# Kernel tuning notes

Hardware: AMD Instinct MI355X
Metric: run time of the kernel (lower is better)

Reference implementation:

```python
import jax, jax.numpy as jnp
import numpy as np

K = 3  # kernel size


def _bilinear_sample(x, px, py):
    """Bilinear sample x:[b,c,h,w] at pixel coords px,py:[b,t,h,w].
    Zeros padding, align_corners=True semantics (coords are raw pixel coords).
    Returns [b,c,t,h,w]."""
    b, c, h, w = x.shape
    x0 = jnp.floor(px)
    y0 = jnp.floor(py)
    wx1 = px - x0
    wx0 = 1.0 - wx1
    wy1 = py - y0
    wy0 = 1.0 - wy1
    xf = x.reshape(b, c, h * w)

    def gather(xi, yi):
        valid = (xi >= 0) & (xi <= w - 1) & (yi >= 0) & (yi <= h - 1)
        xi_c = jnp.clip(xi, 0, w - 1).astype(jnp.int32)
        yi_c = jnp.clip(yi, 0, h - 1).astype(jnp.int32)
        idx = (yi_c * w + xi_c).reshape(b, 1, -1)  # [b,1,t*h*w]
        v = jnp.take_along_axis(xf, idx, axis=2).reshape(b, c, *xi.shape[1:])
        return v * valid[:, None].astype(x.dtype)

    out = (gather(x0, y0) * (wx0 * wy0)[:, None]
           + gather(x0 + 1, y0) * (wx1 * wy0)[:, None]
           + gather(x0, y0 + 1) * (wx0 * wy1)[:, None]
           + gather(x0 + 1, y0 + 1) * (wx1 * wy1)[:, None])
    return out


def setup_inputs() -> dict:
    key = jax.random.key(0)
    k1, k2, k3 = jax.random.split(key, 3)
    b, c, h, w = 4, 64, 128, 128
    out_c = 64
    x = jax.random.normal(k1, (b, c, h, w), dtype=jnp.float32)
    offset = jax.random.normal(k2, (b, 2 * K * K, h, w), dtype=jnp.float32)
    weight = jax.random.normal(k3, (out_c, c, K, K), dtype=jnp.float32) * 0.05
    bias = jnp.zeros((out_c,), dtype=jnp.float32)
    return {"x": x, "offset": offset, "weight": weight, "bias": bias}


def reference(x, offset, weight, bias):
    b, c, h, w = x.shape
    kk = K * K
    # base integer grid (x along width, y along height)
    yy, xx = jnp.meshgrid(jnp.arange(h, dtype=x.dtype), jnp.arange(w, dtype=x.dtype), indexing='ij')
    off = offset.reshape(b, kk, 2, h, w)
    # grid_sample with align_corners=True inverts the module's normalization,
    # so effective sampling coords are simply base + offset in pixel space.
    px = xx[None, None] + off[:, :, 0]  # [b,kk,h,w]
    py = yy[None, None] + off[:, :, 1]
    sampled = _bilinear_sample(x, px, py)  # [b,c,kk,h,w]
    w2 = weight.reshape(weight.shape[0], c, kk)  # [o,c,kk]
    out = jnp.einsum('oct,bcthw->bohw', w2, sampled)
    return out + bias[None, :, None, None]
```

## Files before the change

### kernel.cpp

```cpp
#include <hip/hip_runtime.h>
#include <cstddef>

#define BH 4
#define CH 64
#define OH 64
#define HH 128
#define WW 128
#define KK 9
#define HW (HH * WW)

#define HX 4
#define HYT 4
#define TW 25
#define TH 12
#define NREC (TW * TH)
#define NCHUNK (NREC * 8)

typedef __attribute__((ext_vector_type(8))) short short8;
typedef __attribute__((ext_vector_type(4))) float f32x4;
typedef __attribute__((ext_vector_type(2))) float f32x2;
typedef __attribute__((ext_vector_type(4))) unsigned int uint4v;
typedef __attribute__((ext_vector_type(8))) unsigned short ushort8v;

__device__ __forceinline__ unsigned short f2bf(float f) {
    unsigned u = __float_as_uint(f);
    u += 0x7fffu + ((u >> 16) & 1u);
    return (unsigned short)(u >> 16);
}
__device__ __forceinline__ f32x2 bf2x2(unsigned d) {
    f32x2 r;
    r.x = __uint_as_float(d << 16);
    r.y = __uint_as_float(d & 0xffff0000u);
    return r;
}
__device__ __forceinline__ unsigned pack_bf2(f32x2 v) {
    unsigned u0 = __float_as_uint(v.x);
    u0 += 0x7fffu + ((u0 >> 16) & 1u);
    unsigned u1 = __float_as_uint(v.y);
    u1 += 0x7fffu + ((u1 >> 16) & 1u);
    return __builtin_amdgcn_perm(u1, u0, 0x07060302);
}
__device__ __forceinline__ uint4v combine4(uint4v c00, uint4v c10, uint4v c01, uint4v c11,
                                           float w00, float w10, float w01, float w11) {
    f32x2 W00 = {w00, w00}, W10 = {w10, w10}, W01 = {w01, w01}, W11 = {w11, w11};
    uint4v r;
#pragma unroll
    for (int j = 0; j < 4; ++j) {
        f32x2 s = W00 * bf2x2(c00[j]) + W10 * bf2x2(c10[j])
                + W01 * bf2x2(c01[j]) + W11 * bf2x2(c11[j]);
        r[j] = pack_bf2(s);
    }
    return r;
}

__global__ __launch_bounds__(256) void dcl_prep(const float* __restrict__ x,
                                                const float* __restrict__ wgt,
                                                unsigned short* __restrict__ xt,
                                                unsigned short* __restrict__ wtb) {
    if (blockIdx.x < 1024) {
        __shared__ float tile[64][68];
        int chunk = blockIdx.x;
        int b = chunk >> 8;
        int hw0 = (chunk & 255) * 64;
        int tid = threadIdx.x;
        int cg = tid >> 4;
        int tx4 = (tid & 15) * 4;
        const float* xb = x + (size_t)b * CH * HW + hw0;
#pragma unroll
        for (int pass = 0; pass < 4; ++pass) {
            int c = pass * 16 + cg;
            float4 v = *(const float4*)(xb + (size_t)c * HW + tx4);
            *(float4*)&tile[c][tx4] = v;
        }
        __syncthreads();
        unsigned short* xtb = xt + ((size_t)b << 20) + (size_t)hw0 * CH;
        int c8 = (tid & 7) * 8;
        int p0 = tid >> 3;
#pragma unroll
        for (int it = 0; it < 2; ++it) {
            int pxl = p0 + it * 32;
            ushort8v v;
#pragma unroll
            for (int j = 0; j < 8; ++j) v[j] = f2bf(tile[c8 + j][pxl]);
            *(ushort8v*)(xtb + (size_t)pxl * CH + c8) = v;
        }
    } else {
        int idx = (blockIdx.x - 1024) * 256 + threadIdx.x;
        int j  = idx & 7;
        int l  = (idx >> 3) & 63;
        int nt = (idx >> 9) & 3;
        int ks = idx >> 11;
        int k = ks * 32 + ((l >> 4) * 8) + j;
        int n = nt * 16 + (l & 15);
        int c = k & 63;
        int t = k >> 6;
        wtb[idx] = f2bf(wgt[(n * CH + c) * KK + t]);
    }
}

__global__ __launch_bounds__(256, 4) void dcl_main(
        const unsigned short* __restrict__ xt,
        const float* __restrict__ offset,
        const unsigned short* __restrict__ wtb,
        const float* __restrict__ bias,
        float* __restrict__ out) {
    __shared__ __align__(16) int smem[NREC * 32];
    int tid = threadIdx.x;
    int lane = tid & 63;
    int wave = tid >> 6;

    int b  = blockIdx.x >> 8;
    int t8 = blockIdx.x & 255;
    int x0 = (t8 & 7) << 4;
    int y0 = (t8 >> 3) << 2;
    int m = lane & 15;
    int quad = lane >> 4;
    int qoff = quad * 16;
    int y = y0 + wave;
    int pm = x0 + m;

    const char* xtb = (const char*)xt;
    const char* xim = xtb + (((size_t)b << 14) << 7);
    const float* ob = offset + (((size_t)(b * 18)) << 14) + (y << 7) + pm;
    float pxf = (float)pm;
    float pyf = (float)y;

    float oxv[9], oyv[9];
#pragma unroll
    for (int t = 0; t < 9; ++t) {
        oxv[t] = ob[(size_t)(2 * t) << 14];
        oyv[t] = ob[(size_t)(2 * t + 1) << 14];
    }

    uint4v* sv = (uint4v*)smem;
#pragma unroll
    for (int i = 0; i < 10; ++i) {
        int id = tid + i * 256;
        if (id < NCHUNK) {
            int p = id >> 3, sub = id & 7;
            int r = p / TW, col = p - r * TW;
            int sy = min(max(y0 - HYT + r, 0), HH - 1);
            int sx = min(max(x0 - HX + col, 0), WW - 1);
            uint4v v = *(const uint4v*)(xim + (((sy << 7) + sx) << 7) + (sub << 4));
            sv[p * 8 + ((sub + (p & 7)) & 7)] = v;
        }
    }

    f32x4 acc[4];
#pragma unroll
    for (int i = 0; i < 4; ++i) acc[i] = (f32x4)(0.f);

    const short8* bfrags = (const short8*)wtb;

    __syncthreads();

#pragma unroll
    for (int t = 0; t < 9; ++t) {
        float fx = pxf + oxv[t];
        float fy = pyf + oyv[t];
        float x0f = floorf(fx), y0f = floorf(fy);
        float wx1 = fx - x0f, wy1 = fy - y0f;
        float wx0 = 1.0f - wx1, wy0 = 1.0f - wy1;
        int ix0 = (int)x0f, iy0 = (int)y0f;
        int ix1 = ix0 + 1, iy1 = iy0 + 1;
        bool vx0 = (unsigned)ix0 < (unsigned)WW;
        bool vx1 = (unsigned)ix1 < (unsigned)WW;
        bool vy0 = (unsigned)iy0 < (unsigned)HH;
        bool vy1 = (unsigned)iy1 < (unsigned)HH;
        float w00 = (vx0 && vy0) ? wx0 * wy0 : 0.0f;
        float w10 = (vx1 && vy0) ? wx1 * wy0 : 0.0f;
        float w01 = (vx0 && vy1) ? wx0 * wy1 : 0.0f;
        float w11 = (vx1 && vy1) ? wx1 * wy1 : 0.0f;
        int cx0 = min(max(ix0, 0), WW - 1), cx1 = min(max(ix1, 0), WW - 1);
        int cy0 = min(max(iy0, 0), HH - 1), cy1 = min(max(iy1, 0), HH - 1);

        int lc0 = cx0 - x0 + HX, lc1 = cx1 - x0 + HX;
        int lr0 = cy0 - y0 + HYT, lr1 = cy1 - y0 + HYT;
        bool oof = ((unsigned)lc0 > (TW - 1)) | ((unsigned)lc1 > (TW - 1)) |
                   ((unsigned)lr0 > (TH - 1)) | ((unsigned)lr1 > (TH - 1));
        int sc0 = min(max(lc0, 0), TW - 1), sc1 = min(max(lc1, 0), TW - 1);
        int sr0 = min(max(lr0, 0), TH - 1), sr1 = min(max(lr1, 0), TH - 1);
        int p00 = sr0 * TW + sc0, p10 = sr0 * TW + sc1;
        int p01 = sr1 * TW + sc0, p11 = sr1 * TW + sc1;

        uint4v c00a = sv[p00 * 8 + ((quad + (p00 & 7)) & 7)];
        uint4v c00b = sv[p00 * 8 + ((quad + 4 + (p00 & 7)) & 7)];
        uint4v c10a = sv[p10 * 8 + ((quad + (p10 & 7)) & 7)];
        uint4v c10b = sv[p10 * 8 + ((quad + 4 + (p10 & 7)) & 7)];
        uint4v c01a = sv[p01 * 8 + ((quad + (p01 & 7)) & 7)];
        uint4v c01b = sv[p01 * 8 + ((quad + 4 + (p01 & 7)) & 7)];
        uint4v c11a = sv[p11 * 8 + ((quad + (p11 & 7)) & 7)];
        uint4v c11b = sv[p11 * 8 + ((quad + 4 + (p11 & 7)) & 7)];

        if (__builtin_expect(oof, 0)) {
            int base = b << 14;
            int o00 = ((base + (cy0 << 7) + cx0) << 7) + qoff;
            int o10 = ((base + (cy0 << 7) + cx1) << 7) + qoff;
            int o01 = ((base + (cy1 << 7) + cx0) << 7) + qoff;
            int o11 = ((base + (cy1 << 7) + cx1) << 7) + qoff;
            c00a = *(const uint4v*)(xtb + o00);
            c00b = *(const uint4v*)(xtb + o00 + 64);
            c10a = *(const uint4v*)(xtb + o10);
            c10b = *(const uint4v*)(xtb + o10 + 64);
            c01a = *(const uint4v*)(xtb + o01);
            c01b = *(const uint4v*)(xtb + o01 + 64);
            c11a = *(const uint4v*)(xtb + o11);
            c11b = *(const uint4v*)(xtb + o11 + 64);
        }

        uint4v ra = combine4(c00a, c10a, c01a, c11a, w00, w10, w01, w11);
        uint4v rb = combine4(c00b, c10b, c01b, c11b, w00, w10, w01, w11);
        short8 aa = __builtin_bit_cast(short8, ra);
        short8 ab = __builtin_bit_cast(short8, rb);

        int ks = 2 * t;
#pragma unroll
        for (int nt = 0; nt < 4; ++nt)
            acc[nt] = __builtin_amdgcn_mfma_f32_16x16x32_bf16(
                aa, bfrags[(ks * 4 + nt) * 64 + lane], acc[nt], 0, 0, 0);
#pragma unroll
        for (int nt = 0; nt < 4; ++nt)
            acc[nt] = __builtin_amdgcn_mfma_f32_16x16x32_bf16(
                ab, bfrags[((ks + 1) * 4 + nt) * 64 + lane], acc[nt], 0, 0, 0);
    }

    __syncthreads();
    float* o_w = (float*)smem + wave * 1040;
#pragma unroll
    for (int nt = 0; nt < 4; ++nt)
#pragma unroll
        for (int reg = 0; reg < 4; ++reg)
            o_w[(quad * 4 + reg) * 65 + nt * 16 + m] = acc[nt][reg];
    __syncthreads();

    const float* os = (const float*)smem;
#pragma unroll
    for (int j = tid; j < 64 * 64; j += 256) {
        int o = j >> 6;
        int p = j & 63;
        int row = p >> 4, xx = p & 15;
        float v = os[row * 1040 + xx * 65 + o] + bias[o];
        out[(((size_t)(b * OH + o)) << 14) + ((y0 + row) << 7) + x0 + xx] = v;
    }
}

extern "C" void kernel_launch(void* const* d_in, const int* in_sizes, int n_in,
                              void* d_out, int out_size, void* d_ws, size_t ws_size,
                              hipStream_t stream) {
    const float* x      = (const float*)d_in[0];
    const float* offset = (const float*)d_in[1];
    const float* weight = (const float*)d_in[2];
    const float* bias   = (const float*)d_in[3];
    float* out = (float*)d_out;

    unsigned short* xt  = (unsigned short*)d_ws;
    unsigned short* wtb = (unsigned short*)((char*)d_ws + (size_t)BH * HW * CH * 2);

    dcl_prep<<<1024 + 144, 256, 0, stream>>>(x, weight, xt, wtb);
    dcl_main<<<(BH * HW) / 64, 256, 0, stream>>>(xt, offset, wtb, bias, out);
}
```

Baseline: 101.3 us.

## Process two output rows per wave to reuse weight fragments and halo tile

Each block now covers a 16x8 pixel tile instead of 16x4, and each wave computes two rows with two accumulator sets. Every loaded B (weight) fragment feeds twice as many MFMAs, and the shared-memory halo tile grows from 12 to 16 rows, so halo overhead per output pixel drops. The per-pixel gather is factored into a helper, and offsets are loaded inside the tap loop rather than preloaded. In exchange, register and LDS pressure rise (launch bounds drop to 3 blocks per CU) and the grid halves to 512 blocks, which may reduce occupancy and latency hiding.

```diff
diff --git a/kernel.cpp b/kernel.cpp
--- a/kernel.cpp
+++ b/kernel.cpp
@@ -12,7 +12,7 @@
 #define HX 4
 #define HYT 4
 #define TW 25
-#define TH 12
+#define TH 16
 #define NREC (TW * TH)
 #define NCHUNK (NREC * 8)
 
@@ -50,6 +50,70 @@
                 + W01 * bf2x2(c01[j]) + W11 * bf2x2(c11[j]);
         r[j] = pack_bf2(s);
     }
+    return r;
+}
+
+struct ABfrag { short8 aa, ab; };
+
+__device__ __forceinline__ ABfrag gather_row(
+        const uint4v* sv, const char* xtb, int b, int x0, int y0,
+        float pxf, float pyf, float ox, float oy, int quad) {
+    float fx = pxf + ox;
+    float fy = pyf + oy;
+    float x0f = floorf(fx), y0f = floorf(fy);
+    float wx1 = fx - x0f, wy1 = fy - y0f;
+    float wx0 = 1.0f - wx1, wy0 = 1.0f - wy1;
+    int ix0 = (int)x0f, iy0 = (int)y0f;
+    int ix1 = ix0 + 1, iy1 = iy0 + 1;
+    bool vx0 = (unsigned)ix0 < (unsigned)WW;
+    bool vx1 = (unsigned)ix1 < (unsigned)WW;
+    bool vy0 = (unsigned)iy0 < (unsigned)HH;
+    bool vy1 = (unsigned)iy1 < (unsigned)HH;
+    float w00 = (vx0 && vy0) ? wx0 * wy0 : 0.0f;
+    float w10 = (vx1 && vy0) ? wx1 * wy0 : 0.0f;
+    float w01 = (vx0 && vy1) ? wx0 * wy1 : 0.0f;
+    float w11 = (vx1 && vy1) ? wx1 * wy1 : 0.0f;
+    int cx0 = min(max(ix0, 0), WW - 1), cx1 = min(max(ix1, 0), WW - 1);
+    int cy0 = min(max(iy0, 0), HH - 1), cy1 = min(max(iy1, 0), HH - 1);
+
+    int lc0 = cx0 - x0 + HX, lc1 = cx1 - x0 + HX;
+    int lr0 = cy0 - y0 + HYT, lr1 = cy1 - y0 + HYT;
+    bool oof = ((unsigned)lc0 > (TW - 1)) | ((unsigned)lc1 > (TW - 1)) |
+               ((unsigned)lr0 > (TH - 1)) | ((unsigned)lr1 > (TH - 1));
+    int sc0 = min(max(lc0, 0), TW - 1), sc1 = min(max(lc1, 0), TW - 1);
+    int sr0 = min(max(lr0, 0), TH - 1), sr1 = min(max(lr1, 0), TH - 1);
+    int p00 = sr0 * TW + sc0, p10 = sr0 * TW + sc1;
+    int p01 = sr1 * TW + sc0, p11 = sr1 * TW + sc1;
+
+    uint4v c00a = sv[p00 * 8 + ((quad + (p00 & 7)) & 7)];
+    uint4v c00b = sv[p00 * 8 + ((quad + 4 + (p00 & 7)) & 7)];
+    uint4v c10a = sv[p10 * 8 + ((quad + (p10 & 7)) & 7)];
+    uint4v c10b = sv[p10 * 8 + ((quad + 4 + (p10 & 7)) & 7)];
+    uint4v c01a = sv[p01 * 8 + ((quad + (p01 & 7)) & 7)];
+    uint4v c01b = sv[p01 * 8 + ((quad + 4 + (p01 & 7)) & 7)];
+    uint4v c11a = sv[p11 * 8 + ((quad + (p11 & 7)) & 7)];
+    uint4v c11b = sv[p11 * 8 + ((quad + 4 + (p11 & 7)) & 7)];
+
+    if (__builtin_expect(oof, 0)) {
+        int qoff = quad * 16;
+        int base = b << 14;
+        int o00 = ((base + (cy0 << 7) + cx0) << 7) + qoff;
+        int o10 = ((base + (cy0 << 7) + cx1) << 7) + qoff;
+        int o01 = ((base + (cy1 << 7) + cx0) << 7) + qoff;
+        int o11 = ((base + (cy1 << 7) + cx1) << 7) + qoff;
+        c00a = *(const uint4v*)(xtb + o00);
+        c00b = *(const uint4v*)(xtb + o00 + 64);
+        c10a = *(const uint4v*)(xtb + o10);
+        c10b = *(const uint4v*)(xtb + o10 + 64);
+        c01a = *(const uint4v*)(xtb + o01);
+        c01b = *(const uint4v*)(xtb + o01 + 64);
+        c11a = *(const uint4v*)(xtb + o11);
+        c11b = *(const uint4v*)(xtb + o11 + 64);
+    }
+
+    ABfrag r;
+    r.aa = __builtin_bit_cast(short8, combine4(c00a, c10a, c01a, c11a, w00, w10, w01, w11));
+    r.ab = __builtin_bit_cast(short8, combine4(c00b, c10b, c01b, c11b, w00, w10, w01, w11));
     return r;
 }
 
@@ -98,7 +162,7 @@
     }
 }
 
-__global__ __launch_bounds__(256, 4) void dcl_main(
+__global__ __launch_bounds__(256, 3) void dcl_main(
         const unsigned short* __restrict__ xt,
         const float* __restrict__ offset,
         const unsigned short* __restrict__ wtb,
@@ -109,32 +173,26 @@
     int lane = tid & 63;
     int wave = tid >> 6;
 
-    int b  = blockIdx.x >> 8;
-    int t8 = blockIdx.x & 255;
-    int x0 = (t8 & 7) << 4;
-    int y0 = (t8 >> 3) << 2;
+    int b  = blockIdx.x >> 7;
+    int t7 = blockIdx.x & 127;
+    int x0 = (t7 & 7) << 4;
+    int y0 = (t7 >> 3) << 3;
     int m = lane & 15;
     int quad = lane >> 4;
-    int qoff = quad * 16;
-    int y = y0 + wave;
+    int row0 = y0 + 2 * wave;
     int pm = x0 + m;
 
     const char* xtb = (const char*)xt;
     const char* xim = xtb + (((size_t)b << 14) << 7);
-    const float* ob = offset + (((size_t)(b * 18)) << 14) + (y << 7) + pm;
+    const float* ob0 = offset + (((size_t)(b * 18)) << 14) + (row0 << 7) + pm;
+    const float* ob1 = ob0 + WW;
     float pxf = (float)pm;
-    float pyf = (float)y;
-
-    float oxv[9], oyv[9];
-#pragma unroll
-    for (int t = 0; t < 9; ++t) {
-        oxv[t] = ob[(size_t)(2 * t) << 14];
-        oyv[t] = ob[(size_t)(2 * t + 1) << 14];
-    }
+    float py0 = (float)row0;
+    float py1 = py0 + 1.0f;
 
     uint4v* sv = (uint4v*)smem;
 #pragma unroll
-    for (int i = 0; i < 10; ++i) {
+    for (int i = 0; i < 13; ++i) {
         int id = tid + i * 256;
         if (id < NCHUNK) {
             int p = id >> 3, sub = id & 7;
@@ -146,9 +204,9 @@
         }
     }
 
-    f32x4 acc[4];
-#pragma unroll
-    for (int i = 0; i < 4; ++i) acc[i] = (f32x4)(0.f);
+    f32x4 acc0[4], acc1[4];
+#pragma unroll
+    for (int i = 0; i < 4; ++i) { acc0[i] = (f32x4)(0.f); acc1[i] = (f32x4)(0.f); }
 
     const short8* bfrags = (const short8*)wtb;
 
@@ -156,91 +214,51 @@
 
 #pragma unroll
     for (int t = 0; t < 9; ++t) {
-        float fx = pxf + oxv[t];
-        float fy = pyf + oyv[t];
-        float x0f = floorf(fx), y0f = floorf(fy);
-        float wx1 = fx - x0f, wy1 = fy - y0f;
-        float wx0 = 1.0f - wx1, wy0 = 1.0f - wy1;
-        int ix0 = (int)x0f, iy0 = (int)y0f;
-        int ix1 = ix0 + 1, iy1 = iy0 + 1;
-        bool vx0 = (unsigned)ix0 < (unsigned)WW;
-        bool vx1 = (unsigned)ix1 < (unsigned)WW;
-        bool vy0 = (unsigned)iy0 < (unsigned)HH;
-        bool vy1 = (unsigned)iy1 < (unsigned)HH;
-        float w00 = (vx0 && vy0) ? wx0 * wy0 : 0.0f;
-        float w10 = (vx1 && vy0) ? wx1 * wy0 : 0.0f;
-        float w01 = (vx0 && vy1) ? wx0 * wy1 : 0.0f;
-        float w11 = (vx1 && vy1) ? wx1 * wy1 : 0.0f;
-        int cx0 = min(max(ix0, 0), WW - 1), cx1 = min(max(ix1, 0), WW - 1);
-        int cy0 = min(max(iy0, 0), HH - 1), cy1 = min(max(iy1, 0), HH - 1);
-
-        int lc0 = cx0 - x0 + HX, lc1 = cx1 - x0 + HX;
-        int lr0 = cy0 - y0 + HYT, lr1 = cy1 - y0 + HYT;
-        bool oof = ((unsigned)lc0 > (TW - 1)) | ((unsigned)lc1 > (TW - 1)) |
-                   ((unsigned)lr0 > (TH - 1)) | ((unsigned)lr1 > (TH - 1));
-        int sc0 = min(max(lc0, 0), TW - 1), sc1 = min(max(lc1, 0), TW - 1);
-        int sr0 = min(max(lr0, 0), TH - 1), sr1 = min(max(lr1, 0), TH - 1);
-        int p00 = sr0 * TW + sc0, p10 = sr0 * TW + sc1;
-        int p01 = sr1 * TW + sc0, p11 = sr1 * TW + sc1;
-
-        uint4v c00a = sv[p00 * 8 + ((quad + (p00 & 7)) & 7)];
-        uint4v c00b = sv[p00 * 8 + ((quad + 4 + (p00 & 7)) & 7)];
-        uint4v c10a = sv[p10 * 8 + ((quad + (p10 & 7)) & 7)];
-        uint4v c10b = sv[p10 * 8 + ((quad + 4 + (p10 & 7)) & 7)];
-        uint4v c01a = sv[p01 * 8 + ((quad + (p01 & 7)) & 7)];
-        uint4v c01b = sv[p01 * 8 + ((quad + 4 + (p01 & 7)) & 7)];
-        uint4v c11a = sv[p11 * 8 + ((quad + (p11 & 7)) & 7)];
-        uint4v c11b = sv[p11 * 8 + ((quad + 4 + (p11 & 7)) & 7)];
-
-        if (__builtin_expect(oof, 0)) {
-            int base = b << 14;
-            int o00 = ((base + (cy0 << 7) + cx0) << 7) + qoff;
-            int o10 = ((base + (cy0 << 7) + cx1) << 7) + qoff;
-            int o01 = ((base + (cy1 << 7) + cx0) << 7) + qoff;
-            int o11 = ((base + (cy1 << 7) + cx1) << 7) + qoff;
-            c00a = *(const uint4v*)(xtb + o00);
-            c00b = *(const uint4v*)(xtb + o00 + 64);
-            c10a = *(const uint4v*)(xtb + o10);
-            c10b = *(const uint4v*)(xtb + o10 + 64);
-            c01a = *(const uint4v*)(xtb + o01);
-            c01b = *(const uint4v*)(xtb + o01 + 64);
-            c11a = *(const uint4v*)(xtb + o11);
-            c11b = *(const uint4v*)(xtb + o11 + 64);
-        }
-
-        uint4v ra = combine4(c00a, c10a, c01a, c11a, w00, w10, w01, w11);
-        uint4v rb = combine4(c00b, c10b, c01b, c11b, w00, w10, w01, w11);
-        short8 aa = __builtin_bit_cast(short8, ra);
-        short8 ab = __builtin_bit_cast(short8, rb);
+        float ox0 = ob0[(size_t)(2 * t) << 14];
+        float oy0 = ob0[(size_t)(2 * t + 1) << 14];
+        float ox1 = ob1[(size_t)(2 * t) << 14];
+        float oy1 = ob1[(size_t)(2 * t + 1) << 14];
+
+        ABfrag r0 = gather_row(sv, xtb, b, x0, y0, pxf, py0, ox0, oy0, quad);
+        ABfrag r1 = gather_row(sv, xtb, b, x0, y0, pxf, py1, ox1, oy1, quad);
 
         int ks = 2 * t;
-#pragma unroll
-        for (int nt = 0; nt < 4; ++nt)
-            acc[nt] = __builtin_amdgcn_mfma_f32_16x16x32_bf16(
-                aa, bfrags[(ks * 4 + nt) * 64 + lane], acc[nt], 0, 0, 0);
-#pragma unroll
-        for (int nt = 0; nt < 4; ++nt)
-            acc[nt] = __builtin_amdgcn_mfma_f32_16x16x32_bf16(
-                ab, bfrags[((ks + 1) * 4 + nt) * 64 + lane], acc[nt], 0, 0, 0);
+        short8 bv0[4], bv1[4];
+#pragma unroll
+        for (int nt = 0; nt < 4; ++nt) {
+            bv0[nt] = bfrags[(ks * 4 + nt) * 64 + lane];
+            bv1[nt] = bfrags[((ks + 1) * 4 + nt) * 64 + lane];
+        }
+#pragma unroll
+        for (int nt = 0; nt < 4; ++nt) {
+            acc0[nt] = __builtin_amdgcn_mfma_f32_16x16x32_bf16(r0.aa, bv0[nt], acc0[nt], 0, 0, 0);
+            acc0[nt] = __builtin_amdgcn_mfma_f32_16x16x32_bf16(r0.ab, bv1[nt], acc0[nt], 0, 0, 0);
+            acc1[nt] = __builtin_amdgcn_mfma_f32_16x16x32_bf16(r1.aa, bv0[nt], acc1[nt], 0, 0, 0);
+            acc1[nt] = __builtin_amdgcn_mfma_f32_16x16x32_bf16(r1.ab, bv1[nt], acc1[nt], 0, 0, 0);
+        }
     }
 
     __syncthreads();
-    float* o_w = (float*)smem + wave * 1040;
+    float* o_w = (float*)smem + wave * 2080;
 #pragma unroll
     for (int nt = 0; nt < 4; ++nt)
 #pragma unroll
-        for (int reg = 0; reg < 4; ++reg)
-            o_w[(quad * 4 + reg) * 65 + nt * 16 + m] = acc[nt][reg];
+        for (int reg = 0; reg < 4; ++reg) {
+            o_w[(quad * 4 + reg) * 65 + nt * 16 + m]        = acc0[nt][reg];
+            o_w[(16 + quad * 4 + reg) * 65 + nt * 16 + m]   = acc1[nt][reg];
+        }
     __syncthreads();
 
     const float* os = (const float*)smem;
 #pragma unroll
-    for (int j = tid; j < 64 * 64; j += 256) {
-        int o = j >> 6;
-        int p = j & 63;
-        int row = p >> 4, xx = p & 15;
-        float v = os[row * 1040 + xx * 65 + o] + bias[o];
-        out[(((size_t)(b * OH + o)) << 14) + ((y0 + row) << 7) + x0 + xx] = v;
+    for (int j = tid; j < 64 * 128; j += 256) {
+        int o = j >> 7;
+        int p = j & 127;
+        int w2 = p >> 5, pi = p & 31;
+        int a = pi >> 4, xx = pi & 15;
+        int row = y0 + 2 * w2 + a;
+        float v = os[w2 * 2080 + pi * 65 + o] + bias[o];
+        out[(((size_t)(b * OH + o)) << 14) + (row << 7) + x0 + xx] = v;
     }
 }
 
@@ -257,5 +275,5 @@
     unsigned short* wtb = (unsigned short*)((char*)d_ws + (size_t)BH * HW * CH * 2);
 
     dcl_prep<<<1024 + 144, 256, 0, stream>>>(x, weight, xt, wtb);
-    dcl_main<<<(BH * HW) / 64, 256, 0, stream>>>(xt, offset, wtb, bias, out);
-}
+    dcl_main<<<(BH * HW) / 128, 256, 0, stream>>>(xt, offset, wtb, bias, out);
+}
```

Result: slower. 103.8 us (+2.5%).
